# Performance work log

Measured on AMD Instinct MI355X. Metric: run time of the kernel, lower is better.

The kernel has to match this reference:

```python
import jax, jax.numpy as jnp
import numpy as np

B, T, D = 8, 1024, 1024
H = 16
ATT_DIM = 1024
VAL_DIM = 1024
SCALE = float((D // H) ** 0.5)  # note: uses input_dim//num_heads, not head dim of attention_dim
EPS = 1e-13


def setup_inputs() -> dict:
    key = jax.random.key(0)
    ks = jax.random.split(key, 6)
    inputs = jax.random.normal(ks[0], (B, T, D), dtype=jnp.float32)
    mask = jnp.ones((B, T), dtype=jnp.float32)
    adj = jax.random.uniform(ks[1], (B, T, T), dtype=jnp.float32)
    # combined QKV projection: Linear(D, 2*ATT_DIM + VAL_DIM)
    W_qkv = jax.random.normal(ks[2], (2 * ATT_DIM + VAL_DIM, D), dtype=jnp.float32) * (1.0 / np.sqrt(D))
    b_qkv = jnp.zeros((2 * ATT_DIM + VAL_DIM,), dtype=jnp.float32)
    # output projection: Linear(VAL_DIM, D)
    W_out = jax.random.normal(ks[3], (D, VAL_DIM), dtype=jnp.float32) * (1.0 / np.sqrt(VAL_DIM))
    b_out = jnp.zeros((D,), dtype=jnp.float32)
    return {"inputs": inputs, "mask": mask, "adj": adj,
            "W_qkv": W_qkv, "b_qkv": b_qkv, "W_out": W_out, "b_out": b_out}


def reference(inputs, mask, adj, W_qkv, b_qkv, W_out, b_out):
    b, t, _ = inputs.shape
    dh_a = ATT_DIM // H
    dh_v = VAL_DIM // H
    proj = jnp.einsum('btd,od->bto', inputs, W_qkv) + b_qkv
    q = proj[..., :ATT_DIM]
    k = proj[..., ATT_DIM:2 * ATT_DIM]
    v = proj[..., 2 * ATT_DIM:]
    # [B, H, T, dh]
    q = q.reshape(b, t, H, dh_a).transpose(0, 2, 1, 3)
    k = k.reshape(b, t, H, dh_a).transpose(0, 2, 1, 3)
    v = v.reshape(b, t, H, dh_v).transpose(0, 2, 1, 3)
    scores = jnp.einsum('bhqd,bhkd->bhqk', q, k) / SCALE
    # multiplicative adjacency gate, broadcast over heads
    scores = scores * adj[:, None, :, :]
    # old-allennlp masked_softmax: softmax(scores * mask), re-mask, renormalize
    m = mask[:, None, None, :]  # [B,1,1,T]
    attn = jax.nn.softmax(scores * m, axis=-1)
    attn = attn * m
    attn = attn / (attn.sum(axis=-1, keepdims=True) + EPS)
    out = jnp.einsum('bhqk,bhkd->bhqd', attn, v)  # [B,H,T,dh_v]
    out = out.transpose(0, 2, 1, 3).reshape(b, t, VAL_DIM)
    out = jnp.einsum('btv,ov->bto', out, W_out) + b_out
    return out
```

## Files before the change

### kernel.cpp

```cpp
#include <hip/hip_runtime.h>
#include <hip/hip_bf16.h>
#include <cstdint>


using bf16 = __hip_bfloat16;
typedef __attribute__((ext_vector_type(8))) short short8;
typedef __attribute__((ext_vector_type(4))) short short4v;
typedef __attribute__((ext_vector_type(4))) float floatx4;

#define B_    8
#define T_    1024
#define D_    1024
#define H_    16
#define PROJW 3072

__device__ __forceinline__ void gl2lds16(const void* g, void* l) {
  __builtin_amdgcn_global_load_lds(
      (const __attribute__((address_space(1))) void*)g,
      (__attribute__((address_space(3))) void*)l,
      16, 0, 0);
}

__device__ __forceinline__ unsigned short f2b_bits(float f) {
  return __builtin_bit_cast(unsigned short, __float2bfloat16(f));
}

__global__ __launch_bounds__(256)
void cvt_f32_bf16(const float* __restrict__ src, bf16* __restrict__ dst, int n) {
  int i = (blockIdx.x * 256 + threadIdx.x) * 4;
  if (i < n) {
    floatx4 f = *(const floatx4*)(src + i);
    short4v h;
    h[0] = f2b_bits(f[0]); h[1] = f2b_bits(f[1]);
    h[2] = f2b_bits(f[2]); h[3] = f2b_bits(f[3]);
    *(short4v*)(dst + i) = h;
  }
}

template<int EPI>
__global__ __launch_bounds__(256)
void gemm_bt_bias(const bf16* __restrict__ A, const bf16* __restrict__ Bm,
                  const bf16* __restrict__ bias, void* __restrict__ C0,
                  void* __restrict__ C1, void* __restrict__ C2,
                  int M, int N, int K)
{
  __shared__ __align__(16) unsigned short sA[128 * 64];
  __shared__ __align__(16) unsigned short sB[128 * 64];

  const int tid  = threadIdx.x;
  const int lane = tid & 63;
  const int wv   = tid >> 6;
  const int quad = lane >> 4;
  const int l16  = lane & 15;
  const int wm   = wv >> 1, wn = wv & 1;
  const int bn   = blockIdx.x, bm = blockIdx.y;

  floatx4 acc[4][4];
#pragma unroll
  for (int i = 0; i < 4; ++i)
#pragma unroll
    for (int j = 0; j < 4; ++j) acc[i][j] = (floatx4){0.f, 0.f, 0.f, 0.f};

  const int o_base = wv * 1024 + lane * 16;

  for (int kt = 0; kt < K; kt += 64) {
    __syncthreads();
#pragma unroll
    for (int it = 0; it < 4; ++it) {
      int o = it * 4096 + o_base;
      int row = o >> 7, col = (o & 127) >> 1;
      gl2lds16(A + (size_t)(bm * 128 + row) * K + kt + col,
               &sA[(it * 4096 + wv * 1024) >> 1]);
    }
#pragma unroll
    for (int it = 0; it < 4; ++it) {
      int o = it * 4096 + o_base;
      int row = o >> 7, col = (o & 127) >> 1;
      gl2lds16(Bm + (size_t)(bn * 128 + row) * K + kt + col,
               &sB[(it * 4096 + wv * 1024) >> 1]);
    }
    __syncthreads();

#pragma unroll
    for (int kk = 0; kk < 64; kk += 32) {
      short8 a_[4], b_[4];
#pragma unroll
      for (int i = 0; i < 4; ++i)
        a_[i] = *(const short8*)&sA[(wm * 64 + i * 16 + l16) * 64 + kk + quad * 8];
#pragma unroll
      for (int j = 0; j < 4; ++j)
        b_[j] = *(const short8*)&sB[(wn * 64 + j * 16 + l16) * 64 + kk + quad * 8];
#pragma unroll
      for (int i = 0; i < 4; ++i)
#pragma unroll
        for (int j = 0; j < 4; ++j)
          acc[i][j] = __builtin_amdgcn_mfma_f32_16x16x32_bf16(a_[i], b_[j], acc[i][j], 0, 0, 0);
    }
  }

  if (EPI == 1) {
#pragma unroll
    for (int j = 0; j < 4; ++j) {
      const int colg = bn * 128 + wn * 64 + j * 16 + l16;
      const float bv = __bfloat162float(bias[colg]);
#pragma unroll
      for (int i = 0; i < 4; ++i)
#pragma unroll
        for (int r = 0; r < 4; ++r) {
          int rowg = bm * 128 + wm * 64 + i * 16 + quad * 4 + r;
          ((float*)C0)[(size_t)rowg * N + colg] = acc[i][j][r] + bv;
        }
    }
  } else {
    const int region = bn >> 3;
    if (region < 2) {
      bf16* dst = (bf16*)(region == 0 ? C0 : C1);
#pragma unroll
      for (int j = 0; j < 4; ++j) {
        const int colg = bn * 128 + wn * 64 + j * 16 + l16;
        const int colr = colg & 1023;
        const float bv = __bfloat162float(bias[colg]);
#pragma unroll
        for (int i = 0; i < 4; ++i)
#pragma unroll
          for (int r = 0; r < 4; ++r) {
            int rowg = bm * 128 + wm * 64 + i * 16 + quad * 4 + r;
            dst[(size_t)rowg * 1024 + colr] = __float2bfloat16(acc[i][j][r] + bv);
          }
      }
    } else {
      bf16* vt = (bf16*)C2;
#pragma unroll
      for (int j = 0; j < 4; ++j) {
        const int colg = bn * 128 + wn * 64 + j * 16 + l16;
        const int d  = colg & 63;
        const int hh = (colg >> 6) & 15;
        const float bv = __bfloat162float(bias[colg]);
#pragma unroll
        for (int i = 0; i < 4; ++i) {
          int rowg0 = bm * 128 + wm * 64 + i * 16 + quad * 4;
          int bb = rowg0 >> 10, t0 = rowg0 & 1023;
          short4v pk;
#pragma unroll
          for (int r = 0; r < 4; ++r) pk[r] = (short)f2b_bits(acc[i][j][r] + bv);
          *(short4v*)&vt[((size_t)(bb * 16 + hh) << 16) + ((size_t)d << 10) + t0] = pk;
        }
      }
    }
  }
}

__global__ __launch_bounds__(512)
void attn_fused(const bf16* __restrict__ Qp, const bf16* __restrict__ Kp,
                const bf16* __restrict__ Vt, const float* __restrict__ adj,
                const float* __restrict__ mask, bf16* __restrict__ aout)
{
  __shared__ __align__(16) unsigned short sK[64 * 72];
  __shared__ __align__(16) unsigned short sVT[64 * 72];
  __shared__ __align__(16) unsigned short sP[128 * 72];

  const int tid  = threadIdx.x;
  const int lane = tid & 63;
  const int wv   = tid >> 6;
  const int quad = lane >> 4;
  const int l16  = lane & 15;
  const int h = blockIdx.x, qt = blockIdx.y, b = blockIdx.z;

  const bf16* qbase = Qp + (size_t)(b * T_ + qt * 128 + wv * 16 + l16) * 1024 + h * 64 + quad * 8;
  const short8 aq0 = *(const short8*)qbase;
  const short8 aq1 = *(const short8*)(qbase + 32);

  const int srow  = tid >> 3;
  const int chunk = (tid & 7) * 8;
  const int sig = ((srow & 15) << 2) | (srow >> 4);
  const bf16* kb = Kp + (size_t)(b * T_ + sig) * 1024 + h * 64 + chunk;
  const bf16* vb = Vt + ((size_t)(b * 16 + h) << 16) + ((size_t)srow << 10) + chunk;

  const float* mb = mask + b * T_ + l16 * 4;
  const float* adjr[4];
#pragma unroll
  for (int r = 0; r < 4; ++r)
    adjr[r] = adj + ((size_t)b * T_ + qt * 128 + wv * 16 + quad * 4 + r) * T_ + l16 * 4;

  short8 kr = *(const short8*)kb;
  short8 vr = *(const short8*)vb;

  short8 ones8;
#pragma unroll
  for (int i = 0; i < 8; ++i) ones8[i] = (short)0x3F80;

  floatx4 oacc[4];
#pragma unroll
  for (int d = 0; d < 4; ++d) oacc[d] = (floatx4){0.f, 0.f, 0.f, 0.f};
  floatx4 Lacc = (floatx4){0.f, 0.f, 0.f, 0.f};

  const float SC = 0.125f * 1.44269504088896f;

  for (int kt = 0; kt < 16; ++kt) {
    floatx4 av[4];
    floatx4 mk4 = *(const floatx4*)(mb + kt * 64);
#pragma unroll
    for (int r = 0; r < 4; ++r) av[r] = *(const floatx4*)(adjr[r] + kt * 64);
    float cj[4], off[4];
#pragma unroll
    for (int j = 0; j < 4; ++j) {
      cj[j]  = mk4[j] * SC;
      off[j] = (mk4[j] == 0.f) ? -1e30f : 0.f;
    }

    __syncthreads();
    *(short8*)&sK [srow * 72 + chunk] = kr;
    *(short8*)&sVT[srow * 72 + chunk] = vr;
    __syncthreads();

    {
      int nk = kt < 15 ? kt + 1 : 15;
      kr = *(const short8*)(kb + ((size_t)nk << 16));
      vr = *(const short8*)(vb + (nk << 6));
    }

    floatx4 sacc[4];
#pragma unroll
    for (int j = 0; j < 4; ++j) sacc[j] = (floatx4){0.f, 0.f, 0.f, 0.f};
    __builtin_amdgcn_s_setprio(1);
#pragma unroll
    for (int kk = 0; kk < 64; kk += 32) {
      short8 aq = kk ? aq1 : aq0;
#pragma unroll
      for (int j = 0; j < 4; ++j) {
        short8 bk = *(const short8*)&sK[(j * 16 + l16) * 72 + kk + quad * 8];
        sacc[j] = __builtin_amdgcn_mfma_f32_16x16x32_bf16(aq, bk, sacc[j], 0, 0, 0);
      }
    }
    __builtin_amdgcn_s_setprio(0);

#pragma unroll
    for (int r = 0; r < 4; ++r) {
      short4v ph;
#pragma unroll
      for (int j = 0; j < 4; ++j) {
        float t = sacc[j][r] * av[r][j];
        float z = fminf(fmaf(t, cj[j], off[j]), 100.f);
        float p = exp2f(z);
        unsigned bits = __builtin_bit_cast(unsigned, p);
        ph[j] = (short)((bits + 0x8000u) >> 16);
      }
      *(short4v*)&sP[(wv * 16 + quad * 4 + r) * 72 + l16 * 4] = ph;
    }

    __asm__ __volatile__("" ::: "memory");

    __builtin_amdgcn_s_setprio(1);
#pragma unroll
    for (int kk = 0; kk < 64; kk += 32) {
      short8 ap = *(const short8*)&sP[(wv * 16 + l16) * 72 + kk + quad * 8];
      Lacc = __builtin_amdgcn_mfma_f32_16x16x32_bf16(ap, ones8, Lacc, 0, 0, 0);
#pragma unroll
      for (int d = 0; d < 4; ++d) {
        short8 bv = *(const short8*)&sVT[(d * 16 + l16) * 72 + kk + quad * 8];
        oacc[d] = __builtin_amdgcn_mfma_f32_16x16x32_bf16(ap, bv, oacc[d], 0, 0, 0);
      }
    }
    __builtin_amdgcn_s_setprio(0);
  }

#pragma unroll
  for (int d = 0; d < 4; ++d) {
#pragma unroll
    for (int r = 0; r < 4; ++r) {
      int qrow = qt * 128 + wv * 16 + quad * 4 + r;
      float val = oacc[d][r] / (Lacc[r] + 1e-13f);
      aout[(size_t)(b * T_ + qrow) * 1024 + h * 64 + d * 16 + l16] = __float2bfloat16(val);
    }
  }
}

extern "C" void kernel_launch(void* const* d_in, const int* in_sizes, int n_in,
                              void* d_out, int out_size, void* d_ws, size_t ws_size,
                              hipStream_t stream) {
  const float* inputs = (const float*)d_in[0];
  const float* mask   = (const float*)d_in[1];
  const float* adj    = (const float*)d_in[2];
  const float* W_qkv  = (const float*)d_in[3];
  const float* b_qkv  = (const float*)d_in[4];
  const float* W_out  = (const float*)d_in[5];
  const float* b_out  = (const float*)d_in[6];

  const size_t SEG = (size_t)8192 * 1024;
  bf16* Qp   = (bf16*)d_ws;
  bf16* Kp   = Qp + SEG;
  bf16* Vt   = Kp + SEG;
  bf16* aout = Vt + SEG;
  bf16* wo_bf = Qp;
  bf16* bo_bf = Qp + (size_t)1024 * 1024;

  bf16* ib_bf = (bf16*)d_out;
  bf16* wq_bf = ib_bf + SEG;
  bf16* bq_bf = wq_bf + (size_t)3072 * 1024;

  dim3 blk(256);
  cvt_f32_bf16<<<dim3(8192 * 1024 / 4 / 256), blk, 0, stream>>>(inputs, ib_bf, 8192 * 1024);
  cvt_f32_bf16<<<dim3(3072 * 1024 / 4 / 256), blk, 0, stream>>>(W_qkv, wq_bf, 3072 * 1024);
  cvt_f32_bf16<<<dim3(3), blk, 0, stream>>>(b_qkv, bq_bf, 3072);
  gemm_bt_bias<2><<<dim3(PROJW / 128, (B_ * T_) / 128), blk, 0, stream>>>(
      ib_bf, wq_bf, bq_bf, Qp, Kp, Vt, B_ * T_, PROJW, D_);
  attn_fused<<<dim3(H_, T_ / 128, B_), dim3(512), 0, stream>>>(Qp, Kp, Vt, adj, mask, aout);
  cvt_f32_bf16<<<dim3(1024 * 1024 / 4 / 256), blk, 0, stream>>>(W_out, wo_bf, 1024 * 1024);
  cvt_f32_bf16<<<dim3(1), blk, 0, stream>>>(b_out, bo_bf, 1024);
  gemm_bt_bias<1><<<dim3(D_ / 128, (B_ * T_) / 128), blk, 0, stream>>>(
      aout, wo_bf, bo_bf, d_out, nullptr, nullptr, B_ * T_, D_, D_);
}
```

Baseline: 307.5 us.

## Double-buffer GEMM LDS tiles with swizzled layout and XCD-aware block remap

The projection GEMM now prefetches the next K tile into a second LDS buffer while the MFMA loop runs on the current one, with explicit vmcnt waits and barriers. LDS columns are XOR-swizzled by row to cut bank conflicts on the short8 reads. Block indices are remapped so that consecutive blocks spread across the eight XCDs for better L2 locality. The cost is twice the LDS use, which may reduce occupancy, and a block remap that only covers every block when the grid size is divisible by 8.

Measured after the change: 286.4 us. -6.9%, faster.

```diff
diff --git a/kernel.cpp b/kernel.cpp
--- a/kernel.cpp
+++ b/kernel.cpp
@@ -44,8 +44,8 @@
                   void* __restrict__ C1, void* __restrict__ C2,
                   int M, int N, int K)
 {
-  __shared__ __align__(16) unsigned short sA[128 * 64];
-  __shared__ __align__(16) unsigned short sB[128 * 64];
+  __shared__ __align__(16) unsigned short sA[2][128 * 64];
+  __shared__ __align__(16) unsigned short sB[2][128 * 64];
 
   const int tid  = threadIdx.x;
   const int lane = tid & 63;
@@ -53,7 +53,12 @@
   const int quad = lane >> 4;
   const int l16  = lane & 15;
   const int wm   = wv >> 1, wn = wv & 1;
-  const int bn   = blockIdx.x, bm = blockIdx.y;
+
+  const int gx   = gridDim.x;
+  const int nwg  = gx * gridDim.y;
+  const int bidl = blockIdx.y * gx + blockIdx.x;
+  const int swzb = (bidl & 7) * (nwg >> 3) + (bidl >> 3);
+  const int bn   = swzb % gx, bm = swzb / gx;
 
   floatx4 acc[4][4];
 #pragma unroll
@@ -62,40 +67,62 @@
     for (int j = 0; j < 4; ++j) acc[i][j] = (floatx4){0.f, 0.f, 0.f, 0.f};
 
   const int o_base = wv * 1024 + lane * 16;
-
-  for (int kt = 0; kt < K; kt += 64) {
-    __syncthreads();
-#pragma unroll
-    for (int it = 0; it < 4; ++it) {
-      int o = it * 4096 + o_base;
-      int row = o >> 7, col = (o & 127) >> 1;
-      gl2lds16(A + (size_t)(bm * 128 + row) * K + kt + col,
-               &sA[(it * 4096 + wv * 1024) >> 1]);
-    }
-#pragma unroll
-    for (int it = 0; it < 4; ++it) {
-      int o = it * 4096 + o_base;
-      int row = o >> 7, col = (o & 127) >> 1;
-      gl2lds16(Bm + (size_t)(bn * 128 + row) * K + kt + col,
-               &sB[(it * 4096 + wv * 1024) >> 1]);
-    }
-    __syncthreads();
+  const bf16* gA[4];
+  const bf16* gB[4];
+#pragma unroll
+  for (int it = 0; it < 4; ++it) {
+    int o   = it * 4096 + o_base;
+    int row = o >> 7;
+    int col = ((o & 127) ^ ((row & 7) << 4)) >> 1;
+    gA[it] = A  + (size_t)(bm * 128 + row) * K + col;
+    gB[it] = Bm + (size_t)(bn * 128 + row) * K + col;
+  }
+
+  const int NT = K >> 6;
+#pragma unroll
+  for (int it = 0; it < 4; ++it)
+    gl2lds16(gA[it], &sA[0][(it * 4096 + wv * 1024) >> 1]);
+#pragma unroll
+  for (int it = 0; it < 4; ++it)
+    gl2lds16(gB[it], &sB[0][(it * 4096 + wv * 1024) >> 1]);
+
+  const int swx = (l16 & 7) << 3;
+
+  for (int t = 0; t < NT; ++t) {
+    const int s = t & 1;
+    if (t + 1 < NT) {
+#pragma unroll
+      for (int it = 0; it < 4; ++it)
+        gl2lds16(gA[it] + (size_t)(t + 1) * 64, &sA[s ^ 1][(it * 4096 + wv * 1024) >> 1]);
+#pragma unroll
+      for (int it = 0; it < 4; ++it)
+        gl2lds16(gB[it] + (size_t)(t + 1) * 64, &sB[s ^ 1][(it * 4096 + wv * 1024) >> 1]);
+      __builtin_amdgcn_sched_barrier(0);
+      asm volatile("s_waitcnt vmcnt(8)" ::: "memory");
+    } else {
+      asm volatile("s_waitcnt vmcnt(0)" ::: "memory");
+    }
+    __builtin_amdgcn_s_barrier();
+    __builtin_amdgcn_sched_barrier(0);
 
 #pragma unroll
     for (int kk = 0; kk < 64; kk += 32) {
       short8 a_[4], b_[4];
 #pragma unroll
       for (int i = 0; i < 4; ++i)
-        a_[i] = *(const short8*)&sA[(wm * 64 + i * 16 + l16) * 64 + kk + quad * 8];
+        a_[i] = *(const short8*)&sA[s][(wm * 64 + i * 16 + l16) * 64 + ((kk + quad * 8) ^ swx)];
 #pragma unroll
       for (int j = 0; j < 4; ++j)
-        b_[j] = *(const short8*)&sB[(wn * 64 + j * 16 + l16) * 64 + kk + quad * 8];
+        b_[j] = *(const short8*)&sB[s][(wn * 64 + j * 16 + l16) * 64 + ((kk + quad * 8) ^ swx)];
 #pragma unroll
       for (int i = 0; i < 4; ++i)
 #pragma unroll
         for (int j = 0; j < 4; ++j)
           acc[i][j] = __builtin_amdgcn_mfma_f32_16x16x32_bf16(a_[i], b_[j], acc[i][j], 0, 0, 0);
     }
+
+    __builtin_amdgcn_sched_barrier(0);
+    __builtin_amdgcn_s_barrier();
   }
 
   if (EPI == 1) {
```
